# Kernel tuning notes

Hardware: AMD Instinct MI355X
Metric: run time of the kernel (lower is better)

The kernel has to match this reference:

```python
import jax, jax.numpy as jnp
import numpy as np
from jax import lax

B, L = 2, 2048
DIM, HEADS = 1024, 16
HD = DIM // HEADS            # 64
D_STATE, D_CONV = 16, 4
D_INNER = 2 * DIM            # mamba expand=2
DT_RANK = DIM // 16          # 64


def setup_inputs() -> dict:
    key = jax.random.key(0)
    ks = jax.random.split(key, 12)
    w = lambda k, shape, s=0.02: (jax.random.normal(k, shape, jnp.float32) * s)
    # A initialized as in Mamba: A_log = log(1..d_state) per channel
    A_log = jnp.log(jnp.tile(jnp.arange(1, D_STATE + 1, dtype=jnp.float32), (D_INNER, 1)))
    return {
        "x": jax.random.normal(ks[0], (B, L, DIM), jnp.float32),
        # MultiQueryAttention params (Wqkv: dim -> dim + 2*head_dim)
        "wqkv": w(ks[1], (DIM, DIM + 2 * HD)),
        "bqkv": jnp.zeros((DIM + 2 * HD,), jnp.float32),
        "w_attn_out": w(ks[2], (DIM, DIM)),
        "b_attn_out": jnp.zeros((DIM,), jnp.float32),
        # MambaBlock params
        "w_in": w(ks[3], (DIM, 2 * D_INNER)),          # in_proj (no bias)
        "conv_w": w(ks[4], (D_INNER, D_CONV), 0.1),    # depthwise causal conv
        "conv_b": jnp.zeros((D_INNER,), jnp.float32),
        "w_xproj": w(ks[5], (D_INNER, DT_RANK + 2 * D_STATE)),
        "w_dt": w(ks[6], (DT_RANK, D_INNER)),
        "b_dt": w(ks[7], (D_INNER,), 0.01),
        "A_log": A_log,
        "Dp": jnp.ones((D_INNER,), jnp.float32),
        "w_out": w(ks[8], (D_INNER, DIM)),             # out_proj (no bias)
    }


def _mqa(x, wqkv, bqkv, w_attn_out, b_attn_out):
    b, l, d = x.shape
    qkv = x @ wqkv + bqkv
    q = qkv[..., :DIM].reshape(b, l, HEADS, HD)          # blhd
    k = qkv[..., DIM:DIM + HD]                           # bmd (single shared head)
    v = qkv[..., DIM + HD:]                              # bmd
    scores = jnp.einsum("blhd,bmd->bhlm", q, k) / np.sqrt(HD).astype(np.float32)
    causal = jnp.tril(jnp.ones((l, l), bool))
    scores = jnp.where(causal, scores, jnp.finfo(scores.dtype).min)
    attn = jax.nn.softmax(scores, axis=-1)
    out = jnp.einsum("bhlm,bmd->blhd", attn, v).reshape(b, l, DIM)
    return out @ w_attn_out + b_attn_out


def _mamba(x, w_in, conv_w, conv_b, w_xproj, w_dt, b_dt, A_log, Dp, w_out):
    b, l, d = x.shape
    xr = x @ w_in                                        # (b,l,2*d_inner)
    u0, res = xr[..., :D_INNER], xr[..., D_INNER:]
    # causal depthwise conv1d (torch pads d_conv-1 both sides then slices [:l])
    lhs = u0.transpose(0, 2, 1)                          # (b, d_inner, l)
    rhs = conv_w[:, None, :]                             # (d_inner, 1, d_conv)
    xc = lax.conv_general_dilated(
        lhs, rhs, window_strides=(1,), padding=[(D_CONV - 1, 0)],
        dimension_numbers=("NCH", "OIH", "NCH"), feature_group_count=D_INNER)
    u = jax.nn.silu((xc + conv_b[None, :, None]).transpose(0, 2, 1))  # (b,l,d_inner)

    x_dbl = u @ w_xproj
    delta = jax.nn.softplus(x_dbl[..., :DT_RANK] @ w_dt + b_dt)       # (b,l,d_inner)
    Bm = x_dbl[..., DT_RANK:DT_RANK + D_STATE]                        # (b,l,n)
    Cm = x_dbl[..., DT_RANK + D_STATE:]                               # (b,l,n)
    A = -jnp.exp(A_log)                                               # (d_inner, n)

    def step(h, inp):
        d_t, b_t, c_t, u_t = inp                       # (b,d),(b,n),(b,n),(b,d)
        dA = jnp.exp(d_t[..., None] * A)               # (b,d,n)
        h = dA * h + (d_t * u_t)[..., None] * b_t[:, None, :]
        y = jnp.einsum("bdn,bn->bd", h, c_t)
        return h, y

    xs = (delta.transpose(1, 0, 2), Bm.transpose(1, 0, 2),
          Cm.transpose(1, 0, 2), u.transpose(1, 0, 2))
    h0 = jnp.zeros((b, D_INNER, D_STATE), u.dtype)
    _, ys = lax.scan(step, h0, xs)                     # (l,b,d_inner)
    y = ys.transpose(1, 0, 2) + u * Dp
    y = y * jax.nn.silu(res)
    return y @ w_out


def reference(x, wqkv, bqkv, w_attn_out, b_attn_out, w_in, conv_w, conv_b,
              w_xproj, w_dt, b_dt, A_log, Dp, w_out):
    attended = _mqa(x, wqkv, bqkv, w_attn_out, b_attn_out)
    x1 = attended + x                                   # residual 1
    y = _mamba(x1, w_in, conv_w, conv_b, w_xproj, w_dt, b_dt, A_log, Dp, w_out)
    return y + x1                                       # residual 2
```

## Files before the change

kernel.cpp:

```cpp
#include <hip/hip_runtime.h>

#define L_SEQ   2048
#define BATCH   2
#define NDIM    1024
#define NHEADS  16
#define HD      64
#define DSTATE  16
#define DCONV   4
#define DINNER  2048
#define DTRANK  64
#define CHUNK   32
#define NCHUNK  (L_SEQ / CHUNK)
#define SPLIT_KT 8

typedef short  short8  __attribute__((ext_vector_type(8)));
typedef float  floatx4 __attribute__((ext_vector_type(4)));

#define AS1 __attribute__((address_space(1)))
#define AS3 __attribute__((address_space(3)))

__device__ __forceinline__ float bf2f(ushort u) {
    union { uint i; float f; } v; v.i = ((uint)u) << 16; return v.f;
}
#if defined(__has_builtin) && __has_builtin(__builtin_amdgcn_cvt_pk_bf16_f32)
__device__ __forceinline__ ushort f2bf(float f) {
    auto p = __builtin_amdgcn_cvt_pk_bf16_f32(f, f);
    union { decltype(p) v; ushort u[2]; } cv; cv.v = p;
    return cv.u[0];
}
__device__ __forceinline__ uint pk2bf(float lo, float hi) {
    auto p = __builtin_amdgcn_cvt_pk_bf16_f32(lo, hi);
    union { decltype(p) v; uint u; } cv; cv.v = p;
    return cv.u;
}
#else
__device__ __forceinline__ ushort f2bf(float f) {
    uint x = __float_as_uint(f);
    uint r = (x + 0x7fffu + ((x >> 16) & 1u)) >> 16;
    return (ushort)r;
}
__device__ __forceinline__ uint pk2bf(float lo, float hi) {
    return ((uint)f2bf(hi) << 16) | (uint)f2bf(lo);
}
#endif
__device__ __forceinline__ float silu_f(float x) {
    return x / (1.f + __expf(-x));
}
__device__ __forceinline__ void gld_lds16(const void* g, void* l) {
    __builtin_amdgcn_global_load_lds((const AS1 uint*)g, (AS3 uint*)l, 16, 0, 0);
}
__device__ __forceinline__ float cvt_one(const void* s, int i, int f) {
    return f ? ((const float*)s)[i] : bf2f(((const ushort*)s)[i]);
}

__global__ __launch_bounds__(256) void prep_kernel(
    const void* __restrict__ x_raw,
    const void* __restrict__ wqkv, const void* __restrict__ wao,
    const void* __restrict__ win,  const void* __restrict__ wxp,
    const void* __restrict__ wdt,  const void* __restrict__ wout,
    const void* __restrict__ bqkv, const void* __restrict__ bao,
    const void* __restrict__ convw, const void* __restrict__ convb,
    const void* __restrict__ bdt,  const void* __restrict__ Alog,
    const void* __restrict__ Dp,
    ushort* __restrict__ x_b, ushort* __restrict__ wqkv_t,
    ushort* __restrict__ wao_t, ushort* __restrict__ win_t,
    ushort* __restrict__ wxp_t, ushort* __restrict__ wdt_t,
    ushort* __restrict__ wout_t,
    float* __restrict__ bqkv_f, float* __restrict__ bao_f,
    float* __restrict__ convw_f, float* __restrict__ convb_f,
    float* __restrict__ bdt_f, float* __restrict__ Alog_f,
    float* __restrict__ Dp_f, int* __restrict__ flag)
{
    __shared__ int cnt;
    __shared__ float tile[32][33];
    if (threadIdx.x == 0) cnt = 0;
    __syncthreads();
    {
        ushort w = ((const ushort*)x_raw)[threadIdx.x];
        int e = (w >> 7) & 0xff;
        if (w != 0 && (e < 100 || e > 140)) atomicAdd(&cnt, 1);
    }
    __syncthreads();
    const int f = (cnt >= 16) ? 1 : 0;
    if (blockIdx.x == 0 && threadIdx.x == 0) *flag = f;

    int id = blockIdx.x;
    if (id < 16384) {
        int i = id * 256 + threadIdx.x;
        x_b[i] = f2bf(cvt_one(x_raw, i, f));
        return;
    }
    id -= 16384;

    const void* src = nullptr; ushort* dst = nullptr; int K = 0, N = 0;
    if (id < 1152)                     { src = wqkv; dst = wqkv_t; K = 1024; N = 1152; }
    else if ((id -= 1152) < 1024)      { src = wao;  dst = wao_t;  K = 1024; N = 1024; }
    else if ((id -= 1024) < 4096)      { src = win;  dst = win_t;  K = 1024; N = 4096; }
    else if ((id -= 4096) < 192)       { src = wxp;  dst = wxp_t;  K = 2048; N = 96;   }
    else if ((id -= 192)  < 128)       { src = wdt;  dst = wdt_t;  K = 64;   N = 2048; }
    else if ((id -= 128)  < 2048)      { src = wout; dst = wout_t; K = 2048; N = 1024; }
    else {
        id -= 2048;
        if (id < 256) {
            wxp_t[(size_t)96 * DINNER + id * 256 + threadIdx.x] = 0;
        } else {
            int i = (id - 256) * 256 + threadIdx.x;
            if      (i < 1152)   bqkv_f[i]          = cvt_one(bqkv,  i,          f);
            else if (i < 2176)   bao_f[i - 1152]    = cvt_one(bao,   i - 1152,   f);
            else if (i < 10368)  convw_f[i - 2176]  = cvt_one(convw, i - 2176,   f);
            else if (i < 12416)  convb_f[i - 10368] = cvt_one(convb, i - 10368,  f);
            else if (i < 14464)  bdt_f[i - 12416]   = cvt_one(bdt,   i - 12416,  f);
            else if (i < 47232)  Alog_f[i - 14464]  = -__expf(cvt_one(Alog, i - 14464, f));
            else if (i < 49280)  Dp_f[i - 47232]    = cvt_one(Dp,    i - 47232,  f);
        }
        return;
    }

    const int ntn = N / 32;
    const int n0 = (id % ntn) * 32, k0 = (id / ntn) * 32;
    const int tx = threadIdx.x & 31, ty = threadIdx.x >> 5;
    #pragma unroll
    for (int r = 0; r < 4; ++r) {
        size_t o = (size_t)(k0 + ty + r * 8) * N + n0 + tx;
        tile[ty + r * 8][tx] = cvt_one(src, (int)o, f);
    }
    __syncthreads();
    #pragma unroll
    for (int r = 0; r < 4; ++r) {
        int n = n0 + ty + r * 8;
        dst[(size_t)n * K + k0 + tx] = f2bf(tile[tx][ty + r * 8]);
    }
}

__global__ __launch_bounds__(256) void gemm128(
    const ushort* __restrict__ A, int lda,
    const ushort* __restrict__ Wt,
    const float* __restrict__ bias,
    const ushort* __restrict__ resb,
    ushort* __restrict__ outb, float* __restrict__ outf,
    const int* __restrict__ dtflag,
    int N, int K, int act, int klen, float* __restrict__ psum, int swap)
{
    __shared__ __align__(16) ushort As[128 * 64];
    __shared__ __align__(16) ushort Bs[128 * 64];

    const int tid  = threadIdx.x;
    const int wave = tid >> 6;
    const int lane = tid & 63;
    const int wm = (wave >> 1) * 64;
    const int wn = (wave & 1) * 64;
    const int fm = lane & 15;
    const int quad = lane >> 4;
    const int m0 = (swap ? blockIdx.x : blockIdx.y) * 128;
    const int n0 = (swap ? blockIdx.y : blockIdx.x) * 128;

    floatx4 acc[4][4];
    #pragma unroll
    for (int i = 0; i < 4; ++i)
        #pragma unroll
        for (int j = 0; j < 4; ++j) acc[i][j] = (floatx4){0.f, 0.f, 0.f, 0.f};

    int rowv[4], kgv[4];
    #pragma unroll
    for (int j = 0; j < 4; ++j) {
        int c = wave * 256 + j * 64 + lane;
        rowv[j] = c >> 3;
        kgv[j]  = (((c & 7) ^ ((c >> 3) & 7))) * 8;
    }

    const int kbeg = psum ? (blockIdx.z * klen) : 0;
    const int kend = kbeg + klen;

    for (int k0 = kbeg; k0 < kend; k0 += 64) {
        #pragma unroll
        for (int j = 0; j < 4; ++j)
            gld_lds16(A  + (size_t)(m0 + rowv[j]) * lda + k0 + kgv[j],
                      &As[(wave * 256 + j * 64) * 8]);
        #pragma unroll
        for (int j = 0; j < 4; ++j)
            gld_lds16(Wt + (size_t)(n0 + rowv[j]) * K   + k0 + kgv[j],
                      &Bs[(wave * 256 + j * 64) * 8]);
        __syncthreads();

        #pragma unroll
        for (int h = 0; h < 2; ++h) {
            short8 af[4], bf[4];
            #pragma unroll
            for (int i = 0; i < 4; ++i) {
                int row = wm + i * 16 + fm;
                int slot = (h * 4 + quad) ^ (row & 7);
                af[i] = *(const short8*)&As[row * 64 + slot * 8];
            }
            #pragma unroll
            for (int j = 0; j < 4; ++j) {
                int row = wn + j * 16 + fm;
                int slot = (h * 4 + quad) ^ (row & 7);
                bf[j] = *(const short8*)&Bs[row * 64 + slot * 8];
            }
            #pragma unroll
            for (int i = 0; i < 4; ++i)
                #pragma unroll
                for (int j = 0; j < 4; ++j)
                    acc[i][j] = __builtin_amdgcn_mfma_f32_16x16x32_bf16(af[i], bf[j], acc[i][j], 0, 0, 0);
        }
        __syncthreads();
    }

    if (psum) {
        int mgrid = swap ? gridDim.x : gridDim.y;
        float* po = psum + (size_t)blockIdx.z * ((size_t)mgrid * 128) * N;
        #pragma unroll
        for (int j = 0; j < 4; ++j) {
            int col = n0 + wn + j * 16 + fm;
            #pragma unroll
            for (int i = 0; i < 4; ++i) {
                int rowb = m0 + wm + i * 16 + quad * 4;
                #pragma unroll
                for (int r = 0; r < 4; ++r)
                    po[(size_t)(rowb + r) * N + col] = acc[i][j][r];
            }
        }
        return;
    }

    const int flagv = dtflag ? *dtflag : 0;
    #pragma unroll
    for (int j = 0; j < 4; ++j) {
        int col = n0 + wn + j * 16 + fm;
        float bvv = bias ? bias[col] : 0.f;
        #pragma unroll
        for (int i = 0; i < 4; ++i) {
            int rowb = m0 + wm + i * 16 + quad * 4;
            #pragma unroll
            for (int r = 0; r < 4; ++r) {
                float v = acc[i][j][r] + bvv;
                if (act == 1)
                    v = fmaxf(v, 0.f) + __logf(1.f + __expf(-fabsf(v)));
                size_t o = (size_t)(rowb + r) * N + col;
                if (resb) v += bf2f(resb[o]);
                if (dtflag) {
                    if (flagv) outf[o] = v; else outb[o] = f2bf(v);
                } else {
                    if (outb) outb[o] = f2bf(v);
                    if (outf) outf[o] = v;
                }
            }
        }
    }
}

__global__ __launch_bounds__(256) void combine_xdbl(
    const float* __restrict__ psum, ushort* __restrict__ xdbl)
{
    int idx = blockIdx.x * 256 + threadIdx.x;
    int row = idx / 96, col = idx - row * 96;
    float s = 0.f;
    #pragma unroll
    for (int z = 0; z < 8; ++z)
        s += psum[(size_t)z * 4096 * 128 + row * 128 + col];
    xdbl[idx] = f2bf(s);
}

__global__ __launch_bounds__(256) void flash_attn_split(
    const ushort* __restrict__ qkv, ushort* __restrict__ att,
    ushort* __restrict__ partO, float* __restrict__ partL)
{
    __shared__ __align__(16) ushort Ks[64 * 72];
    __shared__ __align__(16) ushort Vt[64 * 72];

    const int tile = (int)(gridDim.x - 1) - (int)blockIdx.x;
    const int hg   = blockIdx.y;
    const int zz   = blockIdx.z;
    const int b = zz >> 2, s = zz & 3;
    const int q0 = tile * 32;
    const int nkv = (q0 >> 6) + 1;
    const int nsplit = (nkv + SPLIT_KT - 1) / SPLIT_KT;
    if (s >= nsplit) return;
    const int kt0 = s * SPLIT_KT;
    const int kt1 = (nkv < kt0 + SPLIT_KT) ? nkv : (kt0 + SPLIT_KT);

    const int tid  = threadIdx.x;
    const int wave = tid >> 6;
    const int lane = tid & 63;
    const int fm   = lane & 15;
    const int quad = lane >> 4;
    const int h    = hg * 4 + wave;

    const int srow = tid >> 3;
    const int scol = (tid & 7) * 8;
    const int vsw  = (tid & 7) << 3;

    const int addrA = (fm + (quad & 1) * 32) * 4;
    const int addrB = addrA + 64;
    const bool jlo_sel = (quad < 2);

    short8 qf[2][2];
    #pragma unroll
    for (int i = 0; i < 2; ++i)
        #pragma unroll
        for (int kh = 0; kh < 2; ++kh)
            qf[i][kh] = *(const short8*)(qkv +
                (size_t)(b * L_SEQ + q0 + i * 16 + fm) * 1152 + h * HD + kh * 32 + quad * 8);

    floatx4 acc[2][4];
    float l_lane[2];
    #pragma unroll
    for (int i = 0; i < 2; ++i) {
        #pragma unroll
        for (int j = 0; j < 4; ++j) acc[i][j] = (floatx4){0.f, 0.f, 0.f, 0.f};
        l_lane[i] = 0.f;
    }

    short8 kreg[2], vreg[2];
    {
        const int kv0 = kt0 * 64;
        #pragma unroll
        for (int pass = 0; pass < 2; ++pass) {
            int row = srow + pass * 32;
            const ushort* kp = qkv + (size_t)(b * L_SEQ + kv0 + row) * 1152 + NDIM + scol;
            kreg[pass] = *(const short8*)kp;
            vreg[pass] = *(const short8*)(kp + HD);
        }
    }

    for (int kt = kt0; kt < kt1; ++kt) {
        const int kv0 = kt * 64;
        __syncthreads();
        #pragma unroll
        for (int pass = 0; pass < 2; ++pass) {
            int row = srow + pass * 32;
            *(short8*)&Ks[row * 72 + scol] = kreg[pass];
            int mw = row ^ vsw;
            #pragma unroll
            for (int i2 = 0; i2 < 8; ++i2) Vt[(scol + i2) * 72 + mw] = (ushort)vreg[pass][i2];
        }
        __syncthreads();

        if (kt + 1 < kt1) {
            const int kv0n = (kt + 1) * 64;
            #pragma unroll
            for (int pass = 0; pass < 2; ++pass) {
                int row = srow + pass * 32;
                const ushort* kp = qkv + (size_t)(b * L_SEQ + kv0n + row) * 1152 + NDIM + scol;
                kreg[pass] = *(const short8*)kp;
                vreg[pass] = *(const short8*)(kp + HD);
            }
        }

        floatx4 spT[4][2];
        __builtin_amdgcn_s_setprio(1);
        #pragma unroll
        for (int j = 0; j < 4; ++j) {
            short8 kf0 = *(const short8*)&Ks[(j * 16 + fm) * 72 + quad * 8];
            short8 kf1 = *(const short8*)&Ks[(j * 16 + fm) * 72 + 32 + quad * 8];
            #pragma unroll
            for (int i = 0; i < 2; ++i) {
                floatx4 z = (floatx4){0.f, 0.f, 0.f, 0.f};
                z = __builtin_amdgcn_mfma_f32_16x16x32_bf16(kf0, qf[i][0], z, 0, 0, 0);
                z = __builtin_amdgcn_mfma_f32_16x16x32_bf16(kf1, qf[i][1], z, 0, 0, 0);
                spT[j][i] = z;
            }
        }
        __builtin_amdgcn_s_setprio(0);

        const bool diag = (kt == nkv - 1);
        #pragma unroll
        for (int j = 0; j < 4; ++j)
            #pragma unroll
            for (int i = 0; i < 2; ++i) {
                #pragma unroll
                for (int r = 0; r < 4; ++r) {
                    float p = __expf(spT[j][i][r] * 0.125f);
                    if (diag) {
                        int kvg = kv0 + j * 16 + quad * 4 + r;
                        int qg  = q0 + i * 16 + fm;
                        if (kvg > qg) p = 0.f;
                    }
                    spT[j][i][r] = p;
                    l_lane[i] += p;
                }
            }

        uint w0[4][2], w1[4][2];
        #pragma unroll
        for (int j = 0; j < 4; ++j)
            #pragma unroll
            for (int i = 0; i < 2; ++i) {
                w0[j][i] = pk2bf(spT[j][i][0], spT[j][i][1]);
                w1[j][i] = pk2bf(spT[j][i][2], spT[j][i][3]);
            }

        short8 pf[2][2];
        #pragma unroll
        for (int i = 0; i < 2; ++i)
            #pragma unroll
            for (int kh = 0; kh < 2; ++kh) {
                const int jl = kh * 2, jh = kh * 2 + 1;
                uint a0 = (uint)__builtin_amdgcn_ds_bpermute(addrA, (int)w0[jl][i]);
                uint a1 = (uint)__builtin_amdgcn_ds_bpermute(addrA, (int)w0[jh][i]);
                uint b0 = (uint)__builtin_amdgcn_ds_bpermute(addrA, (int)w1[jl][i]);
                uint b1 = (uint)__builtin_amdgcn_ds_bpermute(addrA, (int)w1[jh][i]);
                uint c0 = (uint)__builtin_amdgcn_ds_bpermute(addrB, (int)w0[jl][i]);
                uint c1 = (uint)__builtin_amdgcn_ds_bpermute(addrB, (int)w0[jh][i]);
                uint d0 = (uint)__builtin_amdgcn_ds_bpermute(addrB, (int)w1[jl][i]);
                uint d1 = (uint)__builtin_amdgcn_ds_bpermute(addrB, (int)w1[jh][i]);
                union { uint u[4]; short8 s; } cv;
                cv.u[0] = jlo_sel ? a0 : a1;
                cv.u[1] = jlo_sel ? b0 : b1;
                cv.u[2] = jlo_sel ? c0 : c1;
                cv.u[3] = jlo_sel ? d0 : d1;
                pf[i][kh] = cv.s;
            }

        __builtin_amdgcn_s_setprio(1);
        #pragma unroll
        for (int dj = 0; dj < 4; ++dj) {
            int d = dj * 16 + fm;
            int sw8 = ((d >> 3) & 7) << 3;
            short8 vf0 = *(const short8*)&Vt[d * 72 + ((quad * 8) ^ sw8)];
            short8 vf1 = *(const short8*)&Vt[d * 72 + ((32 + quad * 8) ^ sw8)];
            #pragma unroll
            for (int i = 0; i < 2; ++i) {
                acc[i][dj] = __builtin_amdgcn_mfma_f32_16x16x32_bf16(pf[i][0], vf0, acc[i][dj], 0, 0, 0);
                acc[i][dj] = __builtin_amdgcn_mfma_f32_16x16x32_bf16(pf[i][1], vf1, acc[i][dj], 0, 0, 0);
            }
        }
        __builtin_amdgcn_s_setprio(0);
    }

    #pragma unroll
    for (int i = 0; i < 2; ++i) {
        float rs = l_lane[i];
        rs += __shfl_xor(rs, 16);
        rs += __shfl_xor(rs, 32);
        l_lane[i] = rs;
    }

    if (nsplit == 1) {
        #pragma unroll
        for (int i = 0; i < 2; ++i) {
            float inv[4];
            #pragma unroll
            for (int r = 0; r < 4; ++r)
                inv[r] = 1.f / __shfl(l_lane[i], quad * 4 + r, 16);
            #pragma unroll
            for (int dj = 0; dj < 4; ++dj)
                #pragma unroll
                for (int r = 0; r < 4; ++r) {
                    int q = q0 + i * 16 + quad * 4 + r;
                    att[(size_t)(b * L_SEQ + q) * NDIM + h * HD + dj * 16 + fm] =
                        f2bf(acc[i][dj][r] * inv[r]);
                }
        }
    } else {
        size_t pbase = ((size_t)((s * 2 + b) * 16 + h)) * L_SEQ;
        #pragma unroll
        for (int i = 0; i < 2; ++i)
            #pragma unroll
            for (int dj = 0; dj < 4; ++dj)
                #pragma unroll
                for (int r = 0; r < 4; ++r) {
                    int q = q0 + i * 16 + quad * 4 + r;
                    partO[(pbase + q) * 64 + dj * 16 + fm] = f2bf(acc[i][dj][r]);
                }
        if (lane < 16) {
            #pragma unroll
            for (int i = 0; i < 2; ++i)
                partL[pbase + q0 + i * 16 + fm] = l_lane[i];
        }
    }
}

__global__ __launch_bounds__(256) void attn_combine(
    const ushort* __restrict__ partO, const float* __restrict__ partL,
    ushort* __restrict__ att)
{
    int gid = blockIdx.x * 256 + threadIdx.x;
    int t8 = gid & 7;
    int row = gid >> 3;
    int q  = 512 + (row % 1536);
    int bh = row / 1536;
    int b = bh >> 4, h = bh & 15;
    int nsplit = (((q >> 5) >> 1) + 1 + SPLIT_KT - 1) / SPLIT_KT;

    float sum[8] = {0.f, 0.f, 0.f, 0.f, 0.f, 0.f, 0.f, 0.f};
    float L = 0.f;
    for (int s = 0; s < nsplit; ++s) {
        size_t pbase = ((size_t)((s * 2 + b) * 16 + h)) * L_SEQ + q;
        L += partL[pbase];
        short8 o = *(const short8*)&partO[pbase * 64 + t8 * 8];
        #pragma unroll
        for (int k = 0; k < 8; ++k) sum[k] += bf2f((ushort)o[k]);
    }
    float inv = 1.f / L;
    short8 outv;
    #pragma unroll
    for (int k = 0; k < 8; ++k) outv[k] = (short)f2bf(sum[k] * inv);
    *(short8*)&att[((size_t)(b * L_SEQ + q)) * NDIM + h * HD + t8 * 8] = outv;
}

__global__ __launch_bounds__(256) void conv_silu(
    const ushort* __restrict__ xr, const float* __restrict__ conv_w,
    const float* __restrict__ conv_b, ushort* __restrict__ u)
{
    const int c   = ((blockIdx.x & 7) << 8) + threadIdx.x;
    const int bl0 = (blockIdx.x >> 3) << 4;
    const int l0  = bl0 & (L_SEQ - 1);

    const floatx4 wv = *(const floatx4*)&conv_w[c * DCONV];
    const float bias = conv_b[c];

    float xv[19];
    #pragma unroll
    for (int t = 0; t < 19; ++t) {
        int ls = l0 - 3 + t;
        xv[t] = (ls >= 0)
              ? bf2f(xr[(size_t)(bl0 - 3 + t) * (2 * DINNER) + c])
              : 0.f;
    }

    #pragma unroll
    for (int t = 0; t < 16; ++t) {
        float a = bias + xv[t] * wv[0] + xv[t + 1] * wv[1]
                       + xv[t + 2] * wv[2] + xv[t + 3] * wv[3];
        u[(size_t)(bl0 + t) * DINNER + c] = f2bf(silu_f(a));
    }
}

__global__ __launch_bounds__(256) void scan_phase1(
    const ushort* __restrict__ delta, const ushort* __restrict__ u,
    const ushort* __restrict__ xdbl, const float* __restrict__ negA,
    float* __restrict__ Hend, float* __restrict__ Sdt)
{
    const int idx = blockIdx.x * 256 + threadIdx.x;
    const int d = idx & (DINNER - 1);
    const int b = (idx >> 11) & (BATCH - 1);
    const int c = idx >> 12;

    float Av[DSTATE], h[DSTATE];
    #pragma unroll
    for (int n = 0; n < DSTATE; ++n) {
        Av[n] = negA[d * DSTATE + n];
        h[n] = 0.f;
    }

    const int t0 = c * CHUNK;
    size_t bd = ((size_t)b * L_SEQ + t0) * DINNER + d;
    size_t bx = ((size_t)b * L_SEQ + t0) * 96 + DTRANK;
    float sdt = 0.f;

    for (int t = 0; t < CHUNK; ++t) {
        float dt = bf2f(delta[bd]);
        float uv = bf2f(u[bd]);
        sdt += dt;
        float du = dt * uv;
        short8 B0 = *(const short8*)&xdbl[bx];
        short8 B1 = *(const short8*)&xdbl[bx + 8];
        #pragma unroll
        for (int n = 0; n < 8; ++n)
            h[n] = __expf(dt * Av[n]) * h[n] + du * bf2f((ushort)B0[n]);
        #pragma unroll
        for (int n = 0; n < 8; ++n)
            h[8 + n] = __expf(dt * Av[8 + n]) * h[8 + n] + du * bf2f((ushort)B1[n]);
        bd += DINNER; bx += 96;
    }

    size_t ho = (((size_t)c * BATCH + b) * DINNER + d) * DSTATE;
    #pragma unroll
    for (int n = 0; n < DSTATE; n += 4)
        *(floatx4*)&Hend[ho + n] = (floatx4){h[n], h[n + 1], h[n + 2], h[n + 3]};
    Sdt[((size_t)c * BATCH + b) * DINNER + d] = sdt;
}

__global__ __launch_bounds__(256) void scan_phase2(
    float* __restrict__ H, const float* __restrict__ Sdt,
    const float* __restrict__ negA)
{
    const int idx = blockIdx.x * 256 + threadIdx.x;
    const int n = idx & (DSTATE - 1);
    const int d = (idx >> 4) & (DINNER - 1);
    const int b = idx >> 15;

    const float Av = negA[d * DSTATE + n];
    float hin = 0.f;
    for (int c = 0; c < NCHUNK; ++c) {
        size_t o  = (((size_t)c * BATCH + b) * DINNER + d) * DSTATE + n;
        float e   = H[o];
        float dAc = __expf(Av * Sdt[((size_t)c * BATCH + b) * DINNER + d]);
        H[o] = hin;
        hin = dAc * hin + e;
    }
}

__global__ __launch_bounds__(256) void scan_phase3(
    const ushort* __restrict__ delta, const ushort* __restrict__ u,
    const ushort* __restrict__ xdbl, const float* __restrict__ negA,
    const float* __restrict__ Hin, const float* __restrict__ Dp,
    const ushort* __restrict__ xr, ushort* __restrict__ yb)
{
    const int idx = blockIdx.x * 256 + threadIdx.x;
    const int d = idx & (DINNER - 1);
    const int b = (idx >> 11) & (BATCH - 1);
    const int c = idx >> 12;

    float Av[DSTATE], h[DSTATE];
    size_t ho = (((size_t)c * BATCH + b) * DINNER + d) * DSTATE;
    #pragma unroll
    for (int n = 0; n < DSTATE; n += 4) {
        floatx4 hv = *(const floatx4*)&Hin[ho + n];
        h[n] = hv[0]; h[n + 1] = hv[1]; h[n + 2] = hv[2]; h[n + 3] = hv[3];
    }
    #pragma unroll
    for (int n = 0; n < DSTATE; ++n)
        Av[n] = negA[d * DSTATE + n];

    const float Dpd = Dp[d];
    const int t0 = c * CHUNK;
    size_t bd = ((size_t)b * L_SEQ + t0) * DINNER + d;
    size_t bx = ((size_t)b * L_SEQ + t0) * 96 + DTRANK;
    size_t br = ((size_t)b * L_SEQ + t0) * (2 * DINNER) + DINNER + d;

    for (int t = 0; t < CHUNK; ++t) {
        float dt = bf2f(delta[bd]);
        float uv = bf2f(u[bd]);
        float du = dt * uv;
        short8 B0 = *(const short8*)&xdbl[bx];
        short8 B1 = *(const short8*)&xdbl[bx + 8];
        short8 C0 = *(const short8*)&xdbl[bx + 16];
        short8 C1 = *(const short8*)&xdbl[bx + 24];
        float y = 0.f;
        #pragma unroll
        for (int n = 0; n < 8; ++n) {
            h[n] = __expf(dt * Av[n]) * h[n] + du * bf2f((ushort)B0[n]);
            y += h[n] * bf2f((ushort)C0[n]);
        }
        #pragma unroll
        for (int n = 0; n < 8; ++n) {
            h[8 + n] = __expf(dt * Av[8 + n]) * h[8 + n] + du * bf2f((ushort)B1[n]);
            y += h[8 + n] * bf2f((ushort)C1[n]);
        }
        float yv = y + uv * Dpd;
        float r  = bf2f(xr[br]);
        yb[bd] = f2bf(yv * silu_f(r));
        bd += DINNER; bx += 96; br += 2 * DINNER;
    }
}

extern "C" void kernel_launch(void* const* d_in, const int* in_sizes, int n_in,
                              void* d_out, int out_size, void* d_ws, size_t ws_size,
                              hipStream_t stream) {
    const void* x_raw      = d_in[0];
    const void* wqkv_raw   = d_in[1];
    const void* bqkv_raw   = d_in[2];
    const void* wao_raw    = d_in[3];
    const void* bao_raw    = d_in[4];
    const void* win_raw    = d_in[5];
    const void* convw_raw  = d_in[6];
    const void* convb_raw  = d_in[7];
    const void* wxp_raw    = d_in[8];
    const void* wdt_raw    = d_in[9];
    const void* bdt_raw    = d_in[10];
    const void* Alog_raw   = d_in[11];
    const void* Dp_raw     = d_in[12];
    const void* wout_raw   = d_in[13];

    const int M = BATCH * L_SEQ;

    char* p = (char*)d_ws;
    size_t off = 0;
    auto A_ = [&](size_t bytes) { void* q = p + off; off += (bytes + 255) & ~255ull; return q; };

    ushort* x_b    = (ushort*)A_((size_t)M * NDIM * 2);
    ushort* wqkv_t = (ushort*)A_((size_t)NDIM * 1152 * 2);
    ushort* wao_t  = (ushort*)A_((size_t)NDIM * NDIM * 2);
    ushort* win_t  = (ushort*)A_((size_t)NDIM * 4096 * 2);
    float*  psum   = (float*)x_b;
    ushort* yb     = x_b;
    float*  Sdt    = (float*)(x_b + (size_t)M * DINNER);

    ushort* qkv    = (ushort*)A_((size_t)M * 1152 * 2);
    ushort* att    = (ushort*)A_((size_t)M * NDIM * 2);
    float*  Hend   = (float*)qkv;

    ushort* delta_b = (ushort*)A_((size_t)M * DINNER * 2);

    ushort* wxp_t  = (ushort*)A_((size_t)128 * DINNER * 2);
    ushort* wdt_t  = (ushort*)A_((size_t)DTRANK * DINNER * 2);
    ushort* wout_t = (ushort*)A_((size_t)DINNER * NDIM * 2);
    float*  bqkv_f = (float*)A_(1152 * 4);
    float*  bao_f  = (float*)A_(NDIM * 4);
    float*  convw_f= (float*)A_((size_t)DINNER * DCONV * 4);
    float*  convb_f= (float*)A_(DINNER * 4);
    float*  bdt_f  = (float*)A_(DINNER * 4);
    float*  Alog_f = (float*)A_((size_t)DINNER * DSTATE * 4);
    float*  Dp_f   = (float*)A_(DINNER * 4);
    int*    flag   = (int*)A_(256);
    ushort* x1b    = (ushort*)A_((size_t)M * NDIM * 2);
    ushort* xr     = (ushort*)A_((size_t)M * 4096 * 2);
    ushort* u      = (ushort*)A_((size_t)M * DINNER * 2);
    ushort* xdbl   = (ushort*)A_((size_t)M * 96 * 2);

    ushort* partO = xr;
    float*  partL = (float*)u;

    dim3 blk(256);

    prep_kernel<<<dim3(25473), blk, 0, stream>>>(
        x_raw, wqkv_raw, wao_raw, win_raw, wxp_raw, wdt_raw, wout_raw,
        bqkv_raw, bao_raw, convw_raw, convb_raw, bdt_raw, Alog_raw, Dp_raw,
        x_b, wqkv_t, wao_t, win_t, wxp_t, wdt_t, wout_t,
        bqkv_f, bao_f, convw_f, convb_f, bdt_f, Alog_f, Dp_f, flag);

    gemm128<<<dim3(1152 / 128, M / 128), blk, 0, stream>>>(
        x_b, NDIM, wqkv_t, bqkv_f, nullptr, qkv, nullptr, nullptr, 1152, NDIM, 0, NDIM, nullptr, 0);

    flash_attn_split<<<dim3(L_SEQ / 32, NHEADS / 4, BATCH * 4), blk, 0, stream>>>(
        qkv, att, partO, partL);
    attn_combine<<<dim3(1536), blk, 0, stream>>>(partO, partL, att);

    gemm128<<<dim3(NDIM / 128, M / 128), blk, 0, stream>>>(
        att, NDIM, wao_t, bao_f, x_b, x1b, nullptr, nullptr, NDIM, NDIM, 0, NDIM, nullptr, 0);

    gemm128<<<dim3(M / 128, 4096 / 128), blk, 0, stream>>>(
        x1b, NDIM, win_t, nullptr, nullptr, xr, nullptr, nullptr, 4096, NDIM, 0, NDIM, nullptr, 1);

    conv_silu<<<dim3((M / 16) * (DINNER / 256)), blk, 0, stream>>>(xr, convw_f, convb_f, u);

    gemm128<<<dim3(1, M / 128, 8), blk, 0, stream>>>(
        u, DINNER, wxp_t, nullptr, nullptr, nullptr, nullptr, nullptr, 128, DINNER, 0, DINNER / 8, psum, 0);
    combine_xdbl<<<dim3(M * 96 / 256), blk, 0, stream>>>(psum, xdbl);

    gemm128<<<dim3(DINNER / 128, M / 128), blk, 0, stream>>>(
        xdbl, 96, wdt_t, bdt_f, nullptr, delta_b, nullptr, nullptr, DINNER, DTRANK, 1, DTRANK, nullptr, 0);

    scan_phase1<<<dim3(NCHUNK * BATCH * DINNER / 256), blk, 0, stream>>>(
        delta_b, u, xdbl, Alog_f, Hend, Sdt);
    scan_phase2<<<dim3(BATCH * DINNER * DSTATE / 256), blk, 0, stream>>>(
        Hend, Sdt, Alog_f);
    scan_phase3<<<dim3(NCHUNK * BATCH * DINNER / 256), blk, 0, stream>>>(
        delta_b, u, xdbl, Alog_f, Hend, Dp_f, xr, yb);

    gemm128<<<dim3(M / 128, NDIM / 128), blk, 0, stream>>>(
        yb, DINNER, wout_t, nullptr, x1b, (ushort*)d_out, (float*)d_out, flag, NDIM, DINNER, 0, DINNER, nullptr, 1);
}
```

Measured before the change: 488.5 us.

## Stage GEMM epilogue through LDS for vectorized stores and remap blocks across XCDs

The gemm128 epilogue now writes accumulators into a padded shared-memory tile in two half-passes. Threads then read contiguous 8-element rows and emit 16-byte vector loads of the residual and 16-byte stores of the output, replacing scattered scalar global stores. Block indices are also remapped so consecutive workgroups are spread across the 8 XCDs, aiming for better L2 locality. The change adds two barriers per half-pass and more LDS, and it writes only one of outf/outb when no dtflag is given. The remap also assumes the grid size is a multiple of 8.

```diff
diff --git a/kernel.cpp b/kernel.cpp
--- a/kernel.cpp
+++ b/kernel.cpp
@@ -141,8 +141,9 @@
     const int* __restrict__ dtflag,
     int N, int K, int act, int klen, float* __restrict__ psum, int swap)
 {
-    __shared__ __align__(16) ushort As[128 * 64];
-    __shared__ __align__(16) ushort Bs[128 * 64];
+    __shared__ __align__(16) char smem[34048];
+    ushort* As = (ushort*)smem;
+    ushort* Bs = (ushort*)(smem + 16384);
 
     const int tid  = threadIdx.x;
     const int wave = tid >> 6;
@@ -151,8 +152,18 @@
     const int wn = (wave & 1) * 64;
     const int fm = lane & 15;
     const int quad = lane >> 4;
-    const int m0 = (swap ? blockIdx.x : blockIdx.y) * 128;
-    const int n0 = (swap ? blockIdx.y : blockIdx.x) * 128;
+
+    int bx = blockIdx.x, by = blockIdx.y;
+    {
+        const int gx = gridDim.x;
+        const int nwg = gx * gridDim.y;
+        const int id = by * gx + bx;
+        const int qq = nwg >> 3;
+        const int sid = (id & 7) * qq + (id >> 3);
+        bx = sid % gx; by = sid / gx;
+    }
+    const int m0 = (swap ? bx : by) * 128;
+    const int n0 = (swap ? by : bx) * 128;
 
     floatx4 acc[4][4];
     #pragma unroll
@@ -224,28 +235,52 @@
     }
 
     const int flagv = dtflag ? *dtflag : 0;
-    #pragma unroll
-    for (int j = 0; j < 4; ++j) {
-        int col = n0 + wn + j * 16 + fm;
-        float bvv = bias ? bias[col] : 0.f;
-        #pragma unroll
-        for (int i = 0; i < 4; ++i) {
-            int rowb = m0 + wm + i * 16 + quad * 4;
-            #pragma unroll
-            for (int r = 0; r < 4; ++r) {
-                float v = acc[i][j][r] + bvv;
-                if (act == 1)
-                    v = fmaxf(v, 0.f) + __logf(1.f + __expf(-fabsf(v)));
-                size_t o = (size_t)(rowb + r) * N + col;
-                if (resb) v += bf2f(resb[o]);
-                if (dtflag) {
-                    if (flagv) outf[o] = v; else outb[o] = f2bf(v);
-                } else {
-                    if (outb) outb[o] = f2bf(v);
-                    if (outf) outf[o] = v;
+    const bool wf = dtflag ? (flagv != 0) : (outf != nullptr);
+    float* Cs = (float*)smem;
+    const int lrw = (wm >> 1) + quad * 4;
+    #pragma unroll
+    for (int p = 0; p < 2; ++p) {
+        #pragma unroll
+        for (int ih = 0; ih < 2; ++ih) {
+            const int i = 2 * p + ih;
+            #pragma unroll
+            for (int j = 0; j < 4; ++j) {
+                float bvv = bias ? bias[n0 + wn + j * 16 + fm] : 0.f;
+                #pragma unroll
+                for (int r = 0; r < 4; ++r) {
+                    float v = acc[i][j][r] + bvv;
+                    if (act == 1)
+                        v = fmaxf(v, 0.f) + __logf(1.f + __expf(-fabsf(v)));
+                    Cs[(lrw + ih * 16 + r) * 132 + wn + j * 16 + fm] = v;
                 }
             }
         }
+        __syncthreads();
+        #pragma unroll
+        for (int g = 0; g < 4; ++g) {
+            const int lr   = g * 16 + (tid >> 4);
+            const int colc = (tid & 15) * 8;
+            const int grow = m0 + (lr >> 5) * 64 + (2 * p + ((lr >> 4) & 1)) * 16 + (lr & 15);
+            const size_t o = (size_t)grow * N + n0 + colc;
+            floatx4 v0 = *(const floatx4*)&Cs[lr * 132 + colc];
+            floatx4 v1 = *(const floatx4*)&Cs[lr * 132 + colc + 4];
+            float vv[8] = {v0[0], v0[1], v0[2], v0[3], v1[0], v1[1], v1[2], v1[3]};
+            if (resb) {
+                short8 rs = *(const short8*)&resb[o];
+                #pragma unroll
+                for (int k = 0; k < 8; ++k) vv[k] += bf2f((ushort)rs[k]);
+            }
+            if (wf) {
+                *(floatx4*)&outf[o]     = (floatx4){vv[0], vv[1], vv[2], vv[3]};
+                *(floatx4*)&outf[o + 4] = (floatx4){vv[4], vv[5], vv[6], vv[7]};
+            } else {
+                short8 ov;
+                #pragma unroll
+                for (int k = 0; k < 8; ++k) ov[k] = (short)f2bf(vv[k]);
+                *(short8*)&outb[o] = ov;
+            }
+        }
+        __syncthreads();
     }
 }
 
```

After: 468.0 us. 4.2% less time.
